# Kernel tuning notes

Hardware: AMD Instinct MI355X
Metric: run time of the kernel (lower is better)

## Reference

```python
import jax, jax.numpy as jnp
import numpy as np

N, F_IN, H, C, E = 50000, 512, 128, 64, 800000


def setup_inputs() -> dict:
    key = jax.random.key(0)
    ks = jax.random.split(key, 20)
    stdv = 1.0 / np.sqrt(H)
    std_att = 1.0
    std_att_vec = 1.0 / np.sqrt(3.0)
    u = lambda k, shape, s: jax.random.uniform(k, shape, jnp.float32, -s, s)
    inp = {
        "x": jax.random.normal(ks[0], (N, F_IN), jnp.float32),
        "edge_row": jax.random.randint(ks[1], (E,), 0, N, jnp.int32),
        "edge_col": jax.random.randint(ks[2], (E,), 0, N, jnp.int32),
        "edge_val": jax.random.uniform(ks[3], (E,), jnp.float32) * (1.0 / 16.0),
        "weight_low": u(ks[4], (F_IN, H), stdv),
        "weight_high": u(ks[5], (F_IN, H), stdv),
        "weight_mlp": u(ks[6], (F_IN, H), stdv),
        "att_vec_low": u(ks[7], (H, 1), std_att),
        "att_vec_high": u(ks[8], (H, 1), std_att),
        "att_vec_mlp": u(ks[9], (H, 1), std_att),
        "att_vec": u(ks[10], (3, 3), std_att_vec),
        "weight_low2": u(ks[11], (H, C), stdv),
        "weight_high2": u(ks[12], (H, C), stdv),
        "weight_mlp2": u(ks[13], (H, C), stdv),
        "att_vec_low2": u(ks[14], (C, 1), std_att),
        "att_vec_high2": u(ks[15], (C, 1), std_att),
        "att_vec_mlp2": u(ks[16], (C, 1), std_att),
        "att_vec2": u(ks[17], (3, 3), std_att_vec),
    }
    return inp


def _spmm_low(row, col, val, X):
    # adj_low @ X via gather + segment-sum over edges
    return jax.ops.segment_sum(val[:, None] * X[col], row, num_segments=N)


def _attention(o_low, o_high, o_mlp, a_low, a_high, a_mlp, a_vec):
    T = 3.0
    feats = jnp.concatenate([o_low @ a_low, o_high @ a_high, o_mlp @ a_mlp], axis=1)  # [N,3]
    att = jax.nn.softmax(jax.nn.sigmoid(feats) @ a_vec / T, axis=1)
    return att[:, 0:1], att[:, 1:2], att[:, 2:3]


def _layer(X, row, col, val, W_l, W_h, W_m, a_l, a_h, a_m, a_vec):
    xl = X @ W_l
    xh = X @ W_h
    o_low = jax.nn.relu(_spmm_low(row, col, val, xl))
    o_high = jax.nn.relu(xh - _spmm_low(row, col, val, xh))  # (I - adj_low) @ xh
    o_mlp = jax.nn.relu(X @ W_m)
    al, ah, am = _attention(o_low, o_high, o_mlp, a_l, a_h, a_m, a_vec)
    return 3.0 * (al * o_low + ah * o_high + am * o_mlp)


def reference(x, edge_row, edge_col, edge_val, weight_low, weight_high, weight_mlp,
              att_vec_low, att_vec_high, att_vec_mlp, att_vec,
              weight_low2, weight_high2, weight_mlp2,
              att_vec_low2, att_vec_high2, att_vec_mlp2, att_vec2):
    h = _layer(x, edge_row, edge_col, edge_val, weight_low, weight_high, weight_mlp,
               att_vec_low, att_vec_high, att_vec_mlp, att_vec)
    out = _layer(h, edge_row, edge_col, edge_val, weight_low2, weight_high2, weight_mlp2,
                 att_vec_low2, att_vec_high2, att_vec_mlp2, att_vec2)
    return jax.nn.log_softmax(out, axis=1)
```

## Files before the change

### kernel.cpp

```cpp
#include <hip/hip_runtime.h>
#include <hip/hip_bf16.h>

#define NN 50000
#define F_IN 512
#define HH 128
#define CC 64

typedef __attribute__((ext_vector_type(8))) short short8v;
typedef __attribute__((ext_vector_type(4))) float f32x4;
typedef __attribute__((ext_vector_type(2))) float f32x2;

__device__ __forceinline__ short f2b(float f) {
    unsigned u = __builtin_bit_cast(unsigned, f);
    unsigned r = (u + 0x7fffu + ((u >> 16) & 1u)) >> 16;
    return (short)r;
}
__device__ __forceinline__ float b2f(short s) {
    unsigned u = ((unsigned)(unsigned short)s) << 16;
    return __builtin_bit_cast(float, u);
}
__device__ __forceinline__ float b2f_lo(unsigned p) {
    return __builtin_bit_cast(float, p << 16);
}
__device__ __forceinline__ float b2f_hi(unsigned p) {
    return __builtin_bit_cast(float, p & 0xffff0000u);
}

__device__ __forceinline__ f32x2 q2_lo(unsigned p) {
    return __builtin_amdgcn_cvt_pk_f32_fp8(p, false);
}
__device__ __forceinline__ f32x2 q2_hi(unsigned p) {
    return __builtin_amdgcn_cvt_pk_f32_fp8(p, true);
}

__device__ __forceinline__ int xcd_swz(int bid, int nwg) {
    int q = nwg >> 3, r = nwg & 7;
    int xcd = bid & 7, off = bid >> 3;
    return (xcd < r ? xcd * (q + 1) : r * (q + 1) + (xcd - r) * q) + off;
}

__device__ __forceinline__ void load_lds16(const short* g, short* l) {
    __builtin_amdgcn_global_load_lds(
        (const __attribute__((address_space(1))) unsigned int*)g,
        (__attribute__((address_space(3))) unsigned int*)l,
        16, 0, 0);
}

template <int K, int OUTW>
__device__ __forceinline__ void wprep_body(const float* __restrict__ W0,
                                           const float* __restrict__ W1,
                                           const float* __restrict__ W2,
                                           short* __restrict__ Bt, int id) {
    const int nth = 3 * OUTW * (K / 8);
    if (id >= nth) return;
    const int n = id / (K / 8);
    const int kq = id % (K / 8);
    constexpr int HB = OUTW / 2;
    const int t = n / OUTW;
    const int r = n % OUTW;
    int sel, c;
    if (t < 2) { sel = (r >= HB) ? 1 : 0; c = t * HB + (r % HB); }
    else       { sel = 2; c = r; }
    const float* W = sel == 0 ? W0 : (sel == 1 ? W1 : W2);
    short v[8];
#pragma unroll
    for (int j = 0; j < 8; ++j) v[j] = f2b(W[(size_t)(kq * 8 + j) * OUTW + c]);
#pragma unroll
    for (int j = 0; j < 8; ++j) Bt[(size_t)n * K + kq * 8 + j] = v[j];
}

__global__ __launch_bounds__(256) void prep0(int* __restrict__ counts, int n,
                                             const float* __restrict__ Wl,
                                             const float* __restrict__ Wh,
                                             const float* __restrict__ Wm,
                                             short* __restrict__ Bt1,
                                             const float* __restrict__ Wl2,
                                             const float* __restrict__ Wh2,
                                             const float* __restrict__ Wm2,
                                             short* __restrict__ Bt2,
                                             int nZero, int nW1) {
    const int b = blockIdx.x;
    if (b < nZero) {
        int i = b * 256 + threadIdx.x;
        if (i < n) counts[i] = 0;
    } else if (b < nZero + nW1) {
        wprep_body<F_IN, HH>(Wl, Wh, Wm, Bt1, (b - nZero) * 256 + threadIdx.x);
    } else {
        wprep_body<HH, CC>(Wl2, Wh2, Wm2, Bt2, (b - nZero - nW1) * 256 + threadIdx.x);
    }
}

__global__ __launch_bounds__(256) void hist_xconv(const int* __restrict__ erow,
                                                  int* __restrict__ counts, int E,
                                                  const float* __restrict__ x,
                                                  short* __restrict__ xb, int n8,
                                                  int nHist) {
    const int b = blockIdx.x;
    const int total = gridDim.x;
    const long hb4 = ((long)b * nHist) / total;
    const long ha4 = ((long)(b + 1) * nHist) / total;
    if (ha4 != hb4) {
        int i = (int)hb4 * 256 + threadIdx.x;
        if (i < E) atomicAdd(&counts[erow[i]], 1);
        return;
    }
    int i = (b - (int)hb4) * 256 + threadIdx.x;
    if (i >= n8) return;
    const float4* xp = (const float4*)x;
    const float4 a = xp[2 * i];
    const float4 bb = xp[2 * i + 1];
    short8v o;
    o[0] = f2b(a.x); o[1] = f2b(a.y); o[2] = f2b(a.z); o[3] = f2b(a.w);
    o[4] = f2b(bb.x); o[5] = f2b(bb.y); o[6] = f2b(bb.z); o[7] = f2b(bb.w);
    *reinterpret_cast<short8v*>(&xb[(size_t)i * 8]) = o;
}

template <int K, int BNout>
__device__ __forceinline__ void gemm_body(const short* __restrict__ A,
                                          const short* __restrict__ Bt,
                                          unsigned* __restrict__ xq,
                                          short* __restrict__ xh,
                                          short* __restrict__ xm,
                                          int M, int wg, short* smem) {
    constexpr int BM = 128, BK = 32;
    constexpr int FM = (BNout == 128) ? 4 : 2;
    constexpr int FN = 4;
    constexpr int WM = FM * 16;
    constexpr int NKT = K / BK;
    constexpr int AW = (BM * BK / 512) / 4;
    constexpr int BW_ = (BNout * BK / 512) / 4;
    constexpr int VMC = AW + BW_;
    constexpr int HALF = BM * BK + BNout * BK;
    constexpr int HB = BNout / 2;

    const int tid = threadIdx.x;
    const int lane = tid & 63;
    const int wid = tid >> 6;
    const int bm = wg / 3;
    const int bn = wg % 3;
    const int m0 = bm * BM;
    const int n0 = bn * BNout;
    const int wm = (BNout == 128) ? (wid >> 1) : wid;
    const int wn = (BNout == 128) ? (wid & 1) : 0;

    const int rl = lane >> 2;
    const int sl = (lane & 3) ^ ((lane >> 3) & 3);

    f32x4 acc[FM][FN];
#pragma unroll
    for (int i = 0; i < FM; ++i)
#pragma unroll
        for (int j = 0; j < FN; ++j) acc[i][j] = (f32x4){0.f, 0.f, 0.f, 0.f};

    auto issue = [&](int kt, int b) {
        const int k0 = kt * BK;
        short* As = smem + b * HALF;
        short* Bs = As + BM * BK;
#pragma unroll
        for (int i = 0; i < AW; ++i) {
            int g = wid * AW + i;
            int r = g * 16 + rl;
            int gr = m0 + r; if (gr >= M) gr = M - 1;
            load_lds16(&A[(size_t)gr * K + k0 + sl * 8], &As[g * 512]);
        }
#pragma unroll
        for (int i = 0; i < BW_; ++i) {
            int g = wid * BW_ + i;
            int r = g * 16 + rl;
            load_lds16(&Bt[(size_t)(n0 + r) * K + k0 + sl * 8], &Bs[g * 512]);
        }
    };

    issue(0, 0);

    const int mrow = lane & 15;
    const int kg = lane >> 4;
    for (int kt = 0; kt < NKT; ++kt) {
        const int cur = kt & 1;
        if (kt + 1 < NKT) {
            issue(kt + 1, cur ^ 1);
            asm volatile("s_waitcnt vmcnt(%0)" :: "n"(VMC) : "memory");
        } else {
            asm volatile("s_waitcnt vmcnt(0)" ::: "memory");
        }
        __builtin_amdgcn_s_barrier();
        __builtin_amdgcn_sched_barrier(0);

        const short* As = smem + cur * HALF;
        const short* Bs = As + BM * BK;
        short8v af[FM], bf[FN];
#pragma unroll
        for (int f = 0; f < FM; ++f) {
            int m = wm * WM + f * 16 + mrow;
            af[f] = *reinterpret_cast<const short8v*>(
                &As[m * 32 + ((kg ^ ((m >> 1) & 3)) << 3)]);
        }
#pragma unroll
        for (int f = 0; f < FN; ++f) {
            int nr = wn * 64 + f * 16 + mrow;
            bf[f] = *reinterpret_cast<const short8v*>(
                &Bs[nr * 32 + ((kg ^ ((nr >> 1) & 3)) << 3)]);
        }
#pragma unroll
        for (int i = 0; i < FM; ++i)
#pragma unroll
            for (int j = 0; j < FN; ++j)
                acc[i][j] = __builtin_amdgcn_mfma_f32_16x16x32_bf16(
                    af[i], bf[j], acc[i][j], 0, 0, 0);

        asm volatile("s_waitcnt lgkmcnt(0)" ::: "memory");
        __builtin_amdgcn_sched_barrier(0);
        __builtin_amdgcn_s_barrier();
    }

#pragma unroll
    for (int i = 0; i < FM; ++i)
#pragma unroll
        for (int j = 0; j < FN; ++j) {
            int cc = wn * 64 + j * 16 + (lane & 15);
#pragma unroll
            for (int e = 0; e < 4; ++e) {
                int r = wm * WM + i * 16 + (lane >> 4) * 4 + e;
                smem[r * BNout + cc] = f2b(acc[i][j][e]);
            }
        }
    __syncthreads();

    if (bn == 2) {
        constexpr int CH = BM * BNout / 8;
#pragma unroll
        for (int p = 0; p < CH / 256; ++p) {
            int idx = p * 256 + tid;
            int r = idx / (BNout / 8);
            int c8 = idx % (BNout / 8);
            int grow = m0 + r;
            if (grow < M)
                *reinterpret_cast<int4*>(&xm[(size_t)grow * BNout + c8 * 8]) =
                    *reinterpret_cast<const int4*>(&smem[r * BNout + c8 * 8]);
        }
    } else {
#pragma unroll
        for (int p = 0; p < (BM * (HB / 8)) / 256; ++p) {
            int idx = p * 256 + tid;
            int r = idx / (HB / 8);
            int c8 = idx % (HB / 8);
            int grow = m0 + r;
            if (grow < M)
                *reinterpret_cast<int4*>(&xh[(size_t)grow * BNout + bn * HB + c8 * 8]) =
                    *reinterpret_cast<const int4*>(&smem[r * BNout + HB + c8 * 8]);
        }
#pragma unroll
        for (int p = 0; p < (BM * (BNout / 4)) / 256; ++p) {
            int idx = p * 256 + tid;
            int r = idx / (BNout / 4);
            int k = idx % (BNout / 4);
            int grow = m0 + r;
            if (grow < M) {
                unsigned lw = *reinterpret_cast<const unsigned*>(&smem[r * BNout + 2 * k]);
                unsigned hw = *reinterpret_cast<const unsigned*>(&smem[r * BNout + HB + 2 * k]);
                unsigned w;
                if (BNout == 128) {
                    w = __builtin_amdgcn_cvt_pk_fp8_f32(b2f_lo(lw), b2f_hi(lw), 0, false);
                    w = __builtin_amdgcn_cvt_pk_fp8_f32(b2f_lo(hw), b2f_hi(hw), w, true);
                } else {
                    w = __builtin_amdgcn_cvt_pk_fp8_f32(b2f_lo(lw), b2f_lo(hw), 0, false);
                    w = __builtin_amdgcn_cvt_pk_fp8_f32(b2f_hi(lw), b2f_hi(hw), w, true);
                }
                xq[(size_t)grow * (BNout / 2) + bn * (BNout / 4) + k] = w;
            }
        }
    }
}

template <int BNout>
struct GemmSmem {
    static constexpr int SM1 = 2 * (128 * 32 + BNout * 32);
    static constexpr int SM2 = 128 * BNout;
    static constexpr int SZ = SM1 > SM2 ? SM1 : SM2;
};

template <int K, int BNout>
__global__ __launch_bounds__(256) void gemm_scatter(const short* __restrict__ A,
                                                    const short* __restrict__ Bt,
                                                    unsigned* __restrict__ xq,
                                                    short* __restrict__ xh,
                                                    short* __restrict__ xm,
                                                    int M, int nGemm,
                                                    const int* __restrict__ row,
                                                    const int* __restrict__ col,
                                                    const float* __restrict__ val,
                                                    int* __restrict__ cursor,
                                                    int2* __restrict__ edges, int E,
                                                    int nScat) {
    __shared__ short smem[GemmSmem<BNout>::SZ];

    const int total = nGemm + nScat;
    const int swz = xcd_swz(blockIdx.x, total);
    const long ns_b = ((long)swz * nScat) / total;
    const long ns_a = ((long)(swz + 1) * nScat) / total;

    if (ns_a != ns_b) {
        int i = (int)ns_b * 256 + threadIdx.x;
        if (i < E) {
            int r = row[i];
            int p = atomicAdd(&cursor[r], 1);
            int2 rec;
            rec.x = col[i];
            rec.y = __builtin_bit_cast(int, val[i]);
            edges[p] = rec;
        }
        return;
    }
    gemm_body<K, BNout>(A, Bt, xq, xh, xm, M, swz - (int)ns_b, smem);
}

template <int K, int BNout>
__global__ __launch_bounds__(256) void gemm_mfma(const short* __restrict__ A,
                                                 const short* __restrict__ Bt,
                                                 unsigned* __restrict__ xq,
                                                 short* __restrict__ xh,
                                                 short* __restrict__ xm,
                                                 int M) {
    __shared__ short smem[GemmSmem<BNout>::SZ];
    gemm_body<K, BNout>(A, Bt, xq, xh, xm, M, xcd_swz(blockIdx.x, gridDim.x), smem);
}

__global__ __launch_bounds__(256) void block_sums_kernel(const int* __restrict__ counts,
                                                         int* __restrict__ bsums, int n) {
    __shared__ int s[256];
    int tid = threadIdx.x;
    int i = blockIdx.x * 256 + tid;
    s[tid] = (i < n) ? counts[i] : 0;
    __syncthreads();
#pragma unroll
    for (int off = 128; off > 0; off >>= 1) {
        if (tid < off) s[tid] += s[tid + off];
        __syncthreads();
    }
    if (tid == 0) bsums[blockIdx.x] = s[0];
}

__global__ __launch_bounds__(256) void scan_bsums_kernel(int* __restrict__ bsums, int nb) {
    __shared__ int s[256];
    int t = threadIdx.x;
    int v = (t < nb) ? bsums[t] : 0;
    s[t] = v;
    __syncthreads();
#pragma unroll
    for (int off = 1; off < 256; off <<= 1) {
        int u = (t >= off) ? s[t - off] : 0;
        __syncthreads();
        s[t] += u;
        __syncthreads();
    }
    if (t < nb) bsums[t] = s[t] - v;
}

__global__ __launch_bounds__(256) void scan_final_kernel(const int* __restrict__ counts,
                                                         const int* __restrict__ bsums,
                                                         int* __restrict__ rowptr,
                                                         int* __restrict__ cursor, int n) {
    __shared__ int s[256];
    int tid = threadIdx.x;
    int i = blockIdx.x * 256 + tid;
    int v = (i < n) ? counts[i] : 0;
    s[tid] = v;
    __syncthreads();
#pragma unroll
    for (int off = 1; off < 256; off <<= 1) {
        int t = (tid >= off) ? s[tid - off] : 0;
        __syncthreads();
        s[tid] += t;
        __syncthreads();
    }
    int excl = s[tid] - v + bsums[blockIdx.x];
    if (i < n) {
        rowptr[i] = excl;
        cursor[i] = excl;
        if (i == n - 1) rowptr[n] = excl + v;
    }
}

__device__ __forceinline__ float wave_sum(float v) {
#pragma unroll
    for (int off = 32; off > 0; off >>= 1) v += __shfl_xor(v, off, 64);
    return v;
}
__device__ __forceinline__ float wave_max(float v) {
#pragma unroll
    for (int off = 32; off > 0; off >>= 1) v = fmaxf(v, __shfl_xor(v, off, 64));
    return v;
}

__global__ __launch_bounds__(256) void spmm_att1(const int* __restrict__ rowptr,
                                                 const int2* __restrict__ edges,
                                                 const unsigned* __restrict__ xq,
                                                 const unsigned* __restrict__ xhp,
                                                 const unsigned* __restrict__ xmp,
                                                 const float* __restrict__ a_low,
                                                 const float* __restrict__ a_high,
                                                 const float* __restrict__ a_mlp,
                                                 const float* __restrict__ av,
                                                 short* __restrict__ hb,
                                                 int n) {
    const int node = blockIdx.x * 4 + (threadIdx.x >> 6);
    const int lane = threadIdx.x & 63;
    if (node >= n) return;

    const int s = __builtin_amdgcn_readfirstlane(rowptr[node]);
    const int e = __builtin_amdgcn_readfirstlane(rowptr[node + 1]);

    float l0 = 0.f, l1 = 0.f, h0 = 0.f, h1 = 0.f;
    for (int j = s; j < e; j += 8) {
        int   cq[8];
        float vq[8];
#pragma unroll
        for (int q = 0; q < 8; ++q) {
            const int jj = min(j + q, e - 1);
            const int2 rec = edges[jj];
            cq[q] = __builtin_amdgcn_readfirstlane(rec.x);
            int vb = __builtin_amdgcn_readfirstlane(rec.y);
            float t = __builtin_bit_cast(float, vb);
            vq[q] = (j + q < e) ? t : 0.f;
        }
        unsigned p[8];
#pragma unroll
        for (int q = 0; q < 8; ++q)
            p[q] = xq[(size_t)cq[q] * 64 + lane];
#pragma unroll
        for (int q = 0; q < 8; ++q) {
            const f32x2 lo = q2_lo(p[q]);
            const f32x2 hi = q2_hi(p[q]);
            l0 += vq[q] * lo.x; l1 += vq[q] * lo.y;
            h0 += vq[q] * hi.x; h1 += vq[q] * hi.y;
        }
    }

    const unsigned xhn = xhp[(size_t)node * 64 + lane];
    const unsigned xmn = xmp[(size_t)node * 64 + lane];
    float ol0 = fmaxf(l0, 0.f);
    float ol1 = fmaxf(l1, 0.f);
    float oh0 = fmaxf(b2f_lo(xhn) - h0, 0.f);
    float oh1 = fmaxf(b2f_hi(xhn) - h1, 0.f);
    float om0 = fmaxf(b2f_lo(xmn), 0.f);
    float om1 = fmaxf(b2f_hi(xmn), 0.f);

    const float2 aL = ((const float2*)a_low)[lane];
    const float2 aH = ((const float2*)a_high)[lane];
    const float2 aM = ((const float2*)a_mlp)[lane];
    float dl = wave_sum(ol0 * aL.x + ol1 * aL.y);
    float dh = wave_sum(oh0 * aH.x + oh1 * aH.y);
    float dm = wave_sum(om0 * aM.x + om1 * aM.y);

    const float g0 = 1.f / (1.f + expf(-dl));
    const float g1 = 1.f / (1.f + expf(-dh));
    const float g2 = 1.f / (1.f + expf(-dm));
    float s0 = (g0 * av[0] + g1 * av[3] + g2 * av[6]) * (1.f / 3.f);
    float s1 = (g0 * av[1] + g1 * av[4] + g2 * av[7]) * (1.f / 3.f);
    float s2 = (g0 * av[2] + g1 * av[5] + g2 * av[8]) * (1.f / 3.f);
    float mx = fmaxf(s0, fmaxf(s1, s2));
    float e0 = expf(s0 - mx), e1 = expf(s1 - mx), e2 = expf(s2 - mx);
    float inv = 1.f / (e0 + e1 + e2);
    float at0 = e0 * inv, at1 = e1 * inv, at2 = e2 * inv;

    float ho0 = 3.f * (at0 * ol0 + at1 * oh0 + at2 * om0);
    float ho1 = 3.f * (at0 * ol1 + at1 * oh1 + at2 * om1);
    unsigned pk = (unsigned)(unsigned short)f2b(ho0) |
                  ((unsigned)(unsigned short)f2b(ho1) << 16);
    ((unsigned*)hb)[(size_t)node * 64 + lane] = pk;
}

__global__ __launch_bounds__(256) void spmm_att2(const int* __restrict__ rowptr,
                                                 const int2* __restrict__ edges,
                                                 const unsigned short* __restrict__ xq,
                                                 const short* __restrict__ xhp,
                                                 const short* __restrict__ xmp,
                                                 const float* __restrict__ a_low,
                                                 const float* __restrict__ a_high,
                                                 const float* __restrict__ a_mlp,
                                                 const float* __restrict__ av,
                                                 float* __restrict__ out,
                                                 int n) {
    const int node = blockIdx.x * 4 + (threadIdx.x >> 6);
    const int lane = threadIdx.x & 63;
    if (node >= n) return;

    const int s = __builtin_amdgcn_readfirstlane(rowptr[node]);
    const int e = __builtin_amdgcn_readfirstlane(rowptr[node + 1]);

    float accl = 0.f, acch = 0.f;
    for (int j = s; j < e; j += 8) {
        int   cq[8];
        float vq[8];
#pragma unroll
        for (int q = 0; q < 8; ++q) {
            const int jj = min(j + q, e - 1);
            const int2 rec = edges[jj];
            cq[q] = __builtin_amdgcn_readfirstlane(rec.x);
            int vb = __builtin_amdgcn_readfirstlane(rec.y);
            float t = __builtin_bit_cast(float, vb);
            vq[q] = (j + q < e) ? t : 0.f;
        }
        unsigned short p[8];
#pragma unroll
        for (int q = 0; q < 8; ++q)
            p[q] = xq[(size_t)cq[q] * 64 + lane];
#pragma unroll
        for (int q = 0; q < 8; ++q) {
            const f32x2 d = q2_lo((unsigned)p[q]);
            accl += vq[q] * d.x;
            acch += vq[q] * d.y;
        }
    }

    float ol = fmaxf(accl, 0.f);
    float oh = fmaxf(b2f(xhp[(size_t)node * 64 + lane]) - acch, 0.f);
    float om = fmaxf(b2f(xmp[(size_t)node * 64 + lane]), 0.f);

    float dl = wave_sum(ol * a_low[lane]);
    float dh = wave_sum(oh * a_high[lane]);
    float dm = wave_sum(om * a_mlp[lane]);

    const float g0 = 1.f / (1.f + expf(-dl));
    const float g1 = 1.f / (1.f + expf(-dh));
    const float g2 = 1.f / (1.f + expf(-dm));
    float s0 = (g0 * av[0] + g1 * av[3] + g2 * av[6]) * (1.f / 3.f);
    float s1 = (g0 * av[1] + g1 * av[4] + g2 * av[7]) * (1.f / 3.f);
    float s2 = (g0 * av[2] + g1 * av[5] + g2 * av[8]) * (1.f / 3.f);
    float mx3 = fmaxf(s0, fmaxf(s1, s2));
    float e0 = expf(s0 - mx3), e1 = expf(s1 - mx3), e2 = expf(s2 - mx3);
    float inv = 1.f / (e0 + e1 + e2);
    float at0 = e0 * inv, at1 = e1 * inv, at2 = e2 * inv;

    float o = 3.f * (at0 * ol + at1 * oh + at2 * om);

    float m = wave_max(o);
    float ex = expf(o - m);
    float su = wave_sum(ex);
    out[(size_t)node * 64 + lane] = o - m - logf(su);
}

extern "C" void kernel_launch(void* const* d_in, const int* in_sizes, int n_in,
                              void* d_out, int out_size, void* d_ws, size_t ws_size,
                              hipStream_t stream) {
    const float* x    = (const float*)d_in[0];
    const int*   erow = (const int*)d_in[1];
    const int*   ecol = (const int*)d_in[2];
    const float* eval = (const float*)d_in[3];
    const float* Wl   = (const float*)d_in[4];
    const float* Wh   = (const float*)d_in[5];
    const float* Wm   = (const float*)d_in[6];
    const float* al   = (const float*)d_in[7];
    const float* ah   = (const float*)d_in[8];
    const float* am   = (const float*)d_in[9];
    const float* av   = (const float*)d_in[10];
    const float* Wl2  = (const float*)d_in[11];
    const float* Wh2  = (const float*)d_in[12];
    const float* Wm2  = (const float*)d_in[13];
    const float* al2  = (const float*)d_in[14];
    const float* ah2  = (const float*)d_in[15];
    const float* am2  = (const float*)d_in[16];
    const float* av2  = (const float*)d_in[17];
    float* out = (float*)d_out;

    const int E = in_sizes[1];
    const int N = NN;

    short* ws    = (short*)d_ws;
    short* xb    = ws;
    short* xh1   = xb + (size_t)N * 512;
    short* xm1   = xh1 + (size_t)N * 128;
    short* hb    = xm1 + (size_t)N * 128;
    unsigned* xq1 = (unsigned*)(hb + (size_t)N * 128);
    short* Bt1   = (short*)(xq1 + (size_t)N * 64);
    short* Bt2   = Bt1 + 384 * 512;
    int*   ip    = (int*)(Bt2 + 192 * 128);
    int*   counts = ip;
    int*   rowptr = ip + N;
    int*   cursor = ip + 2 * N + 1;
    int*   bsums  = ip + 3 * N + 1;
    int2*  edges  = (int2*)(((size_t)(ip + 3 * N + 1 + 256) + 15) & ~(size_t)15);

    unsigned* xq2 = xq1;
    short* xh2 = xh1;
    short* xm2 = xh1 + (size_t)N * 64;

    const int NB = (N + 255) / 256;
    const int EB = (E + 255) / 256;
    const int node_blocks = (N + 3) / 4;
    const int MT = (N + 127) / 128;
    const int XCB = (N * F_IN / 8 + 255) / 256;
    const int W1B = (3 * HH * (F_IN / 8) + 255) / 256;
    const int W2B = (3 * CC * (HH / 8) + 255) / 256;
    const int nGemm1 = MT * 3;

    prep0<<<NB + W1B + W2B, 256, 0, stream>>>(counts, N, Wl, Wh, Wm, Bt1,
                                              Wl2, Wh2, Wm2, Bt2, NB, W1B);
    hist_xconv<<<EB + XCB, 256, 0, stream>>>(erow, counts, E, x, xb,
                                             N * F_IN / 8, EB);
    block_sums_kernel<<<NB, 256, 0, stream>>>(counts, bsums, N);
    scan_bsums_kernel<<<1, 256, 0, stream>>>(bsums, NB);
    scan_final_kernel<<<NB, 256, 0, stream>>>(counts, bsums, rowptr, cursor, N);

    gemm_scatter<F_IN, HH><<<nGemm1 + EB, 256, 0, stream>>>(
        xb, Bt1, xq1, xh1, xm1, N, nGemm1, erow, ecol, eval, cursor, edges, E, EB);
    spmm_att1<<<node_blocks, 256, 0, stream>>>(rowptr, edges, xq1,
                                               (const unsigned*)xh1,
                                               (const unsigned*)xm1,
                                               al, ah, am, av, hb, N);

    gemm_mfma<HH, CC><<<MT * 3, 256, 0, stream>>>(hb, Bt2, xq2, xh2, xm2, N);
    spmm_att2<<<node_blocks, 256, 0, stream>>>(rowptr, edges,
                                               (const unsigned short*)xq2,
                                               xh2, xm2,
                                               al2, ah2, am2, av2, out, N);
}
```

Baseline: 195.1 us.

## Triple-buffer GEMM LDS pipeline and partition edge scatter by row range

The GEMM main loop moves from double to triple buffering, keeping two K-tiles of loads in flight and issuing the next load after the compute barrier. MFMA issue is wrapped in s_setprio to favour the matrix work. The edge scatter blocks now each handle a slice of one of eight row ranges, so each block reads eight chunks of edges and only scatters those whose row falls in its range. The aim is better locality for the cursor atomics and the edge writes. The cost is more LDS per block, which can lower occupancy, and the edge arrays are read eight times over.

```diff
diff --git a/kernel.cpp b/kernel.cpp
--- a/kernel.cpp
+++ b/kernel.cpp
@@ -172,21 +172,22 @@
     };
 
     issue(0, 0);
+    issue(1, 1);
+    issue(2, 2);
 
     const int mrow = lane & 15;
     const int kg = lane >> 4;
     for (int kt = 0; kt < NKT; ++kt) {
-        const int cur = kt & 1;
-        if (kt + 1 < NKT) {
-            issue(kt + 1, cur ^ 1);
+        if (kt + 2 < NKT)
+            asm volatile("s_waitcnt vmcnt(%0)" :: "n"(2 * VMC) : "memory");
+        else if (kt + 1 < NKT)
             asm volatile("s_waitcnt vmcnt(%0)" :: "n"(VMC) : "memory");
-        } else {
+        else
             asm volatile("s_waitcnt vmcnt(0)" ::: "memory");
-        }
         __builtin_amdgcn_s_barrier();
         __builtin_amdgcn_sched_barrier(0);
 
-        const short* As = smem + cur * HALF;
+        const short* As = smem + (kt % 3) * HALF;
         const short* Bs = As + BM * BK;
         short8v af[FM], bf[FN];
 #pragma unroll
@@ -201,16 +202,19 @@
             bf[f] = *reinterpret_cast<const short8v*>(
                 &Bs[nr * 32 + ((kg ^ ((nr >> 1) & 3)) << 3)]);
         }
+        __builtin_amdgcn_s_setprio(1);
 #pragma unroll
         for (int i = 0; i < FM; ++i)
 #pragma unroll
             for (int j = 0; j < FN; ++j)
                 acc[i][j] = __builtin_amdgcn_mfma_f32_16x16x32_bf16(
                     af[i], bf[j], acc[i][j], 0, 0, 0);
+        __builtin_amdgcn_s_setprio(0);
 
         asm volatile("s_waitcnt lgkmcnt(0)" ::: "memory");
         __builtin_amdgcn_sched_barrier(0);
         __builtin_amdgcn_s_barrier();
+        if (kt + 3 < NKT) issue(kt + 3, kt % 3);
     }
 
 #pragma unroll
@@ -274,7 +278,7 @@
 
 template <int BNout>
 struct GemmSmem {
-    static constexpr int SM1 = 2 * (128 * 32 + BNout * 32);
+    static constexpr int SM1 = 3 * (128 * 32 + BNout * 32);
     static constexpr int SM2 = 128 * BNout;
     static constexpr int SZ = SM1 > SM2 ? SM1 : SM2;
 };
@@ -300,14 +304,25 @@
     const long ns_a = ((long)(swz + 1) * nScat) / total;
 
     if (ns_a != ns_b) {
-        int i = (int)ns_b * 256 + threadIdx.x;
-        if (i < E) {
-            int r = row[i];
-            int p = atomicAdd(&cursor[r], 1);
-            int2 rec;
-            rec.x = col[i];
-            rec.y = __builtin_bit_cast(int, val[i]);
-            edges[p] = rec;
+        const int ns = (int)ns_b;
+        const int SL = nScat >> 3;
+        const int s = ns / SL;
+        const int l = ns % SL;
+        const int rlo = s * (NN / 8);
+        const int rhi = rlo + (NN / 8);
+#pragma unroll
+        for (int c = 0; c < 8; ++c) {
+            int i = (l * 8 + c) * 256 + (int)threadIdx.x;
+            if (i < E) {
+                int r = row[i];
+                if (r >= rlo && r < rhi) {
+                    int p = atomicAdd(&cursor[r], 1);
+                    int2 rec;
+                    rec.x = col[i];
+                    rec.y = __builtin_bit_cast(int, val[i]);
+                    edges[p] = rec;
+                }
+            }
         }
         return;
     }
@@ -593,6 +608,7 @@
     const int W1B = (3 * HH * (F_IN / 8) + 255) / 256;
     const int W2B = (3 * CC * (HH / 8) + 255) / 256;
     const int nGemm1 = MT * 3;
+    const int nScat = ((EB + 7) / 8) * 8;
 
     prep0<<<NB + W1B + W2B, 256, 0, stream>>>(counts, N, Wl, Wh, Wm, Bt1,
                                               Wl2, Wh2, Wm2, Bt2, NB, W1B);
@@ -602,8 +618,8 @@
     scan_bsums_kernel<<<1, 256, 0, stream>>>(bsums, NB);
     scan_final_kernel<<<NB, 256, 0, stream>>>(counts, bsums, rowptr, cursor, N);
 
-    gemm_scatter<F_IN, HH><<<nGemm1 + EB, 256, 0, stream>>>(
-        xb, Bt1, xq1, xh1, xm1, N, nGemm1, erow, ecol, eval, cursor, edges, E, EB);
+    gemm_scatter<F_IN, HH><<<nGemm1 + nScat, 256, 0, stream>>>(
+        xb, Bt1, xq1, xh1, xm1, N, nGemm1, erow, ecol, eval, cursor, edges, E, nScat);
     spmm_att1<<<node_blocks, 256, 0, stream>>>(rowptr, edges, xq1,
                                                (const unsigned*)xh1,
                                                (const unsigned*)xm1,
```

Result: slower. 208.9 us (+7.1%).
